# Performance work log

Measured on AMD Instinct MI355X. Metric: run time of the kernel, lower is better.

## Reference

```python
import jax, jax.numpy as jnp
import numpy as np
import math

STEP_SIZE = 1.0


def setup_inputs() -> dict:
    key = jax.random.key(0)
    ks = jax.random.split(key, 6)
    B, L, C, H, O = 4096, 256, 8, 128, 1
    n_int = L - 1
    coeffs = jax.random.normal(ks[0], (B, n_int, 4 * C), dtype=jnp.float32) * 0.1

    def lin(k, i, o):
        kw, kb = jax.random.split(k)
        s = 1.0 / math.sqrt(i)
        W = jax.random.uniform(kw, (i, o), minval=-s, maxval=s, dtype=jnp.float32)
        b = jax.random.uniform(kb, (o,), minval=-s, maxval=s, dtype=jnp.float32)
        return W, b

    W_init, b_init = lin(ks[1], C, H)
    W1, b1 = lin(ks[2], H, H)
    W2, b2 = lin(ks[3], H, H)
    W3, b3 = lin(ks[4], H, H * C)
    W_out, b_out = lin(ks[5], H, O)
    return dict(coeffs=coeffs, W_init=W_init, b_init=b_init, W1=W1, b1=b1,
                W2=W2, b2=b2, W3=W3, b3=b3, W_out=W_out, b_out=b_out)


def reference(coeffs, W_init, b_init, W1, b1, W2, b2, W3, b3, W_out, b_out):
    B, n_int, four_c = coeffs.shape
    C = four_c // 4
    H = W1.shape[0]
    # torchcde CubicSpline coefficient layout: a, b, two_c, three_d
    a, bcoef, two_c, three_d = jnp.split(coeffs, 4, axis=-1)  # each (B, n_int, C)
    knots = jnp.arange(n_int + 1, dtype=coeffs.dtype)  # t = linspace(0, n_int, n_int+1)
    T = float(n_int)

    def X_deriv(t):
        # torchcde _interpret_t: bucketize(t, knots)-1 clamped; here knots uniform
        idx = jnp.clip(jnp.searchsorted(knots, t, side='left') - 1, 0, n_int - 1)
        frac = t - knots[idx]
        return bcoef[:, idx] + (two_c[:, idx] + three_d[:, idx] * frac) * frac  # (B, C)

    def ode_f(t, z):
        # CDEFunc: Linear->Softplus x2, Linear->Tanh, reshape to (B, H, C)
        h = jax.nn.softplus(z @ W1 + b1)
        h = jax.nn.softplus(h @ W2 + b2)
        f = jnp.tanh(h @ W3 + b3).reshape(B, H, C)
        return jnp.einsum('bhc,bc->bh', f, X_deriv(t))  # f(z) @ dX/dt

    # torchdiffeq fixed-grid rk4 with step_size (3/8 rule: rk4_alt_step_func)
    n_steps = int(math.ceil(T / STEP_SIZE))
    ts = jnp.minimum(jnp.arange(n_steps + 1, dtype=coeffs.dtype) * STEP_SIZE, T)
    t0s, dts = ts[:-1], ts[1:] - ts[:-1]

    z0 = a[:, 0] @ W_init + b_init  # X.evaluate(interval[0]) == a at first knot

    def step(z, td):
        t0, dt = td
        k1 = ode_f(t0, z)
        k2 = ode_f(t0 + dt / 3, z + dt * k1 / 3)
        k3 = ode_f(t0 + dt * 2 / 3, z + dt * (k2 - k1 / 3))
        k4 = ode_f(t0 + dt, z + dt * (k1 - k2 + k3))
        return z + dt * (k1 + 3.0 * (k2 + k3) + k4) / 8.0, None

    zT, _ = jax.lax.scan(step, z0, (t0s, dts))
    return zT @ W_out + b_out
```

## Files before the change

### kernel.cpp

```cpp
#include <hip/hip_runtime.h>

#define NINT  255
#define BM    16
#define PITCH 136

typedef __bf16 bf16x8 __attribute__((ext_vector_type(8)));
typedef float  f32x4  __attribute__((ext_vector_type(4)));

#define MFMA(a, b, c) __builtin_amdgcn_mfma_f32_16x16x32_bf16((a), (b), (c), 0, 0, 0)

__device__ __forceinline__ unsigned short f2b(float f) {
    __bf16 b = (__bf16)f;
    return __builtin_bit_cast(unsigned short, b);
}

__device__ __forceinline__ float sp_f(float x) {
    float e = __builtin_amdgcn_exp2f(x * 1.4426950408889634f);
    float y = __builtin_amdgcn_logf(1.0f + e) * 0.6931471805599453f;
    return (x > 80.0f) ? x : y;
}

__device__ __forceinline__ float tanh_f(float x) {
    float e = __builtin_amdgcn_exp2f(x * 2.8853900817779268f);
    float r = __builtin_amdgcn_rcpf(e + 1.0f);
    return fmaf(-2.0f, r, 1.0f);
}

__global__ void prep_frags(const float* __restrict__ W1, const float* __restrict__ W2,
                           const float* __restrict__ W3,
                           unsigned short* __restrict__ W1f, unsigned short* __restrict__ W2f,
                           unsigned short* __restrict__ W3f) {
    const int e = blockIdx.x * 256 + threadIdx.x;
    const int i = e & 7;
    const int l = (e >> 3) & 63;
    const int t = (e >> 9) & 3;
    const int n = e >> 11;
    const int k = 32 * t + ((l >> 4) & 3) * 8 + i;
    const int c = l & 15;
    if (e < 16384) {
        W1f[e] = f2b(W1[k * 128 + 16 * n + c]);
        W2f[e] = f2b(W2[k * 128 + 16 * n + c]);
    }
    W3f[e] = f2b(W3[k * 1024 + 16 * n + c]);
}

#define RK_UPDATE(ST, JL)                                                        \
{                                                                                \
    float znew;                                                                  \
    if (ST == 0)      { k1r[JL] = p; znew = zb[JL] + p * (1.0f/3.0f); }          \
    else if (ST == 1) { k2r[JL] = p; znew = zb[JL] + p - k1r[JL] * (1.0f/3.0f); }\
    else if (ST == 2) { k3r[JL] = p; znew = zb[JL] + k1r[JL] - k2r[JL] + p; }    \
    else { zb[JL] = fmaf(k1r[JL] + 3.0f*(k2r[JL] + k3r[JL]) + p, 0.125f, zb[JL]); znew = zb[JL]; } \
    if ((g & 1) == 0)                                                            \
        Zs[l15 * PITCH + 32 * JL + h2wb] = f2b(znew);                            \
}

#define STAGE_BODY(ST)                                                           \
{                                                                                \
    if (w < 8) {                                                                 \
        bf16x8 a0[4];                                                            \
        _Pragma("unroll") for (int t = 0; t < 4; ++t)                            \
            a0[t] = *(const bf16x8*)(Zs + l15 * PITCH + t * 32 + koff);          \
        f32x4 h1 = {b1r, b1r, b1r, b1r};                                         \
        _Pragma("unroll") for (int t = 0; t < 4; ++t)                            \
            h1 = MFMA(a0[t], w12r[t], h1);                                       \
        _Pragma("unroll") for (int t = 0; t < 4; ++t)                            \
            w12r[t] = w2v[(w * 4 + t) * 64 + l];               \
        _Pragma("unroll") for (int i = 0; i < 4; ++i)                            \
            H1s[(g * 4 + i) * PITCH + 16 * w + l15] = f2b(sp_f(h1[i]));          \
    }                                                                            \
    __syncthreads();                                                             \
    if (w < 8) {                                                                 \
        bf16x8 a1[4];                                                            \
        _Pragma("unroll") for (int t = 0; t < 4; ++t)                            \
            a1[t] = *(const bf16x8*)(H1s + l15 * PITCH + t * 32 + koff);         \
        f32x4 h2 = {b2r, b2r, b2r, b2r};                                         \
        _Pragma("unroll") for (int t = 0; t < 4; ++t)                            \
            h2 = MFMA(a1[t], w12r[t], h2);                                       \
        _Pragma("unroll") for (int t = 0; t < 4; ++t)                            \
            w12r[t] = w1v[(w * 4 + t) * 64 + l];            \
        _Pragma("unroll") for (int i = 0; i < 4; ++i)                            \
            H2s[(g * 4 + i) * PITCH + 16 * w + l15] = f2b(sp_f(h2[i]));          \
    }                                                                            \
    __syncthreads();                                                             \
    {                                                                            \
        bf16x8 bfr[4];                                                           \
        _Pragma("unroll") for (int t = 0; t < 4; ++t)                            \
            bfr[t] = *(const bf16x8*)(H2s + l15 * PITCH + t * 32 + koff);        \
        const f32x4 xdv = *(const f32x4*)&Xds[par][ST][l15][chB];                \
                                           \
        {                                                                        \
            f32x4 acc0 = *(const f32x4*)&b3s[16 * w + 4 * g];                    \
            f32x4 acc1 = *(const f32x4*)&b3s[16 * (16 + w) + 4 * g];             \
            _Pragma("unroll") for (int t = 0; t < 4; ++t) {                      \
                acc0 = MFMA(w3g[0][t], bfr[t], acc0);                            \
                acc1 = MFMA(w3g[1][t], bfr[t], acc1);                            \
            }                                                                    \
            float p;                                                             \
            p = 0.0f;                                                            \
            _Pragma("unroll") for (int i = 0; i < 4; ++i)                        \
                p = fmaf(tanh_f(acc0[i]), xdv[i], p);                            \
            p += __shfl_xor(p, 16, 64);                                          \
            RK_UPDATE(ST, 0)                                                     \
            p = 0.0f;                                                            \
            _Pragma("unroll") for (int i = 0; i < 4; ++i)                        \
                p = fmaf(tanh_f(acc1[i]), xdv[i], p);                            \
            p += __shfl_xor(p, 16, 64);                                          \
            RK_UPDATE(ST, 1)                                                     \
        }                                                                        \
                     \
        {                                                                        \
            f32x4 acc0 = *(const f32x4*)&b3s[16 * (32 + w) + 4 * g];             \
            f32x4 acc1 = *(const f32x4*)&b3s[16 * (48 + w) + 4 * g];             \
            _Pragma("unroll") for (int t = 0; t < 4; ++t) {                      \
                acc0 = MFMA(w3lv[(w * 4 + t) * 64 + l], bfr[t], acc0);           \
                acc1 = MFMA(w3lv[((16 + w) * 4 + t) * 64 + l], bfr[t], acc1);    \
            }                                                                    \
            float p;                                                             \
            p = 0.0f;                                                            \
            _Pragma("unroll") for (int i = 0; i < 4; ++i)                        \
                p = fmaf(tanh_f(acc0[i]), xdv[i], p);                            \
            p += __shfl_xor(p, 16, 64);                                          \
            RK_UPDATE(ST, 2)                                                     \
            p = 0.0f;                                                            \
            _Pragma("unroll") for (int i = 0; i < 4; ++i)                        \
                p = fmaf(tanh_f(acc1[i]), xdv[i], p);                            \
            p += __shfl_xor(p, 16, 64);                                          \
            RK_UPDATE(ST, 3)                                                     \
        }                                                                        \
    }                                                                            \
    __syncthreads();                                                             \
}

__global__ __launch_bounds__(1024, 4)
void cde_mfma(const float* __restrict__ coeffs,
              const float* __restrict__ W_init, const float* __restrict__ b_init,
              const float* __restrict__ b1, const float* __restrict__ b2,
              const float* __restrict__ b3,
              const float* __restrict__ W_out, const float* __restrict__ b_out,
              const unsigned short* __restrict__ w1f, const unsigned short* __restrict__ w2f,
              const unsigned short* __restrict__ w3f,
              float* __restrict__ out)
{
    __shared__ __align__(16) unsigned short W3l_lds[65536];
    __shared__ __align__(16) unsigned short Zs [BM * PITCH];
    __shared__ __align__(16) unsigned short H1s[BM * PITCH];
    __shared__ __align__(16) unsigned short H2s[BM * PITCH];
    __shared__ __align__(16) float b3s[1024];
    __shared__ __align__(16) float Xds[2][4][16][8];
    __shared__ __align__(16) float Outp[32][16];

    const int tid     = threadIdx.x;
    const int rowbase = blockIdx.x * BM;
    const int l       = tid & 63;
    const int w       = tid >> 6;
    const int l15     = l & 15;
    const int g       = (l >> 4) & 3;
    const int hb      = g >> 1;
    const int koff    = g * 8;
    const int chB     = 4 * (g & 1);
    const int h2wb    = 2 * w + hb;

    for (int k4 = tid; k4 < 8192; k4 += 1024)
        ((uint4*)W3l_lds)[k4] = ((const uint4*)(w3f + 32 * 2048))[k4];
    b3s[tid] = b3[tid];

    const bf16x8* w1v = (const bf16x8*)w1f;
    const bf16x8* w2v = (const bf16x8*)w2f;
    const bf16x8* w3v = (const bf16x8*)w3f;
    bf16x8 w3g[2][4];
    #pragma unroll
    for (int jl = 0; jl < 2; ++jl)
        #pragma unroll
        for (int t = 0; t < 4; ++t)
            w3g[jl][t] = w3v[((16 * jl + w) * 4 + t) * 64 + l];

    bf16x8 w12r[4];
    float b1r = 0.0f, b2r = 0.0f;
    if (w < 8) {
        #pragma unroll
        for (int t = 0; t < 4; ++t)
            w12r[t] = w1v[(w * 4 + t) * 64 + l];
        b1r = b1[16 * w + l15];
        b2r = b2[16 * w + l15];
    }

    float zb[4], k1r[4], k2r[4], k3r[4];
    {
        const float* ap = coeffs + (size_t)(rowbase + l15) * (NINT * 32);
        float av[8];
        #pragma unroll
        for (int c = 0; c < 8; ++c) av[c] = ap[c];
        #pragma unroll
        for (int jl = 0; jl < 4; ++jl) {
            const int h = 32 * jl + h2wb;
            float z = b_init[h];
            #pragma unroll
            for (int c = 0; c < 8; ++c) z = fmaf(av[c], W_init[c * 128 + h], z);
            zb[jl] = z;
            if ((g & 1) == 0) Zs[l15 * PITCH + h] = f2b(z);
        }
    }

    const bf16x8* w3lv = (const bf16x8*)W3l_lds;
    __syncthreads();

    #pragma unroll 1
    for (int step = 0; step < NINT; ++step) {
        const int par = step & 1;
        if (tid < 128) {
            const int m = tid >> 3, c = tid & 7;
            const float* cp = coeffs + (size_t)(rowbase + m) * (NINT * 32);
            float s1;
            if (step == 0) s1 = cp[8 + c];
            else {
                const int i0 = (step - 1) * 32;
                s1 = cp[i0 + 8 + c] + cp[i0 + 16 + c] + cp[i0 + 24 + c];
            }
            const int ik = step * 32;
            const float bB = cp[ik + 8 + c];
            const float tc = cp[ik + 16 + c];
            const float td = cp[ik + 24 + c];
            Xds[par][0][m][c] = s1;
            Xds[par][1][m][c] = bB + (tc + td * (1.0f/3.0f)) * (1.0f/3.0f);
            Xds[par][2][m][c] = bB + (tc + td * (2.0f/3.0f)) * (2.0f/3.0f);
            Xds[par][3][m][c] = bB + tc + td;
        }

        STAGE_BODY(0)
        STAGE_BODY(1)
        STAGE_BODY(2)
        STAGE_BODY(3)
    }

    if ((g & 1) == 0) {
        float prt = 0.0f;
        #pragma unroll
        for (int jl = 0; jl < 4; ++jl)
            prt = fmaf(zb[jl], W_out[32 * jl + h2wb], prt);
        Outp[h2wb][l15] = prt;
    }
    __syncthreads();
    if (tid < 16) {
        float s = b_out[0];
        #pragma unroll
        for (int p = 0; p < 32; ++p) s += Outp[p][tid];
        out[rowbase + tid] = s;
    }
}

extern "C" void kernel_launch(void* const* d_in, const int* in_sizes, int n_in,
                              void* d_out, int out_size, void* d_ws, size_t ws_size,
                              hipStream_t stream) {
    const float* coeffs = (const float*)d_in[0];
    const float* W_init = (const float*)d_in[1];
    const float* b_init = (const float*)d_in[2];
    const float* W1     = (const float*)d_in[3];
    const float* b1     = (const float*)d_in[4];
    const float* W2     = (const float*)d_in[5];
    const float* b2     = (const float*)d_in[6];
    const float* W3     = (const float*)d_in[7];
    const float* b3     = (const float*)d_in[8];
    const float* W_out  = (const float*)d_in[9];
    const float* b_out  = (const float*)d_in[10];
    float* outp = (float*)d_out;

    unsigned short* w1f = (unsigned short*)d_ws;
    unsigned short* w2f = w1f + 16384;
    unsigned short* w3f = w2f + 16384;

    hipLaunchKernelGGL(prep_frags, dim3(512), dim3(256), 0, stream, W1, W2, W3, w1f, w2f, w3f);
    hipLaunchKernelGGL(cde_mfma, dim3(4096 / BM), dim3(1024), 0, stream,
                       coeffs, W_init, b_init, b1, b2, b3, W_out, b_out,
                       w1f, w2f, w3f, outp);
}
```

Baseline: 3.069 ms.

## Shrink block to 12 waves and redistribute W3 tiles unevenly across waves

The block drops from 16 to 12 wavefronts (768 threads). The 64 W3 output tiles are now spread across the waves, with waves 0-3 handling 6 tiles and the rest 5. Each wave holds 3 register-resident W3 fragment groups instead of 2; tiles 32 and up still read from LDS. This is meant to cut per-block scheduling and barrier overhead and raise per-wave work, at the cost of load imbalance, more registers per wave, and fewer waves to hide latency.

Measured after the change: 2.907 ms. 5.3% less time.

```diff
diff --git a/kernel.cpp b/kernel.cpp
--- a/kernel.cpp
+++ b/kernel.cpp
@@ -44,15 +44,15 @@
     W3f[e] = f2b(W3[k * 1024 + 16 * n + c]);
 }
 
-#define RK_UPDATE(ST, JL)                                                        \
+#define RK_UPDATE(ST, T, TILE)                                                   \
 {                                                                                \
     float znew;                                                                  \
-    if (ST == 0)      { k1r[JL] = p; znew = zb[JL] + p * (1.0f/3.0f); }          \
-    else if (ST == 1) { k2r[JL] = p; znew = zb[JL] + p - k1r[JL] * (1.0f/3.0f); }\
-    else if (ST == 2) { k3r[JL] = p; znew = zb[JL] + k1r[JL] - k2r[JL] + p; }    \
-    else { zb[JL] = fmaf(k1r[JL] + 3.0f*(k2r[JL] + k3r[JL]) + p, 0.125f, zb[JL]); znew = zb[JL]; } \
+    if (ST == 0)      { k1r[T] = p; znew = zb[T] + p * (1.0f/3.0f); }            \
+    else if (ST == 1) { k2r[T] = p; znew = zb[T] + p - k1r[T] * (1.0f/3.0f); }   \
+    else if (ST == 2) { k3r[T] = p; znew = zb[T] + k1r[T] - k2r[T] + p; }        \
+    else { zb[T] = fmaf(k1r[T] + 3.0f*(k2r[T] + k3r[T]) + p, 0.125f, zb[T]); znew = zb[T]; } \
     if ((g & 1) == 0)                                                            \
-        Zs[l15 * PITCH + 32 * JL + h2wb] = f2b(znew);                            \
+        Zs[l15 * PITCH + 2 * (TILE) + hb] = f2b(znew);                           \
 }
 
 #define STAGE_BODY(ST)                                                           \
@@ -88,51 +88,30 @@
         _Pragma("unroll") for (int t = 0; t < 4; ++t)                            \
             bfr[t] = *(const bf16x8*)(H2s + l15 * PITCH + t * 32 + koff);        \
         const f32x4 xdv = *(const f32x4*)&Xds[par][ST][l15][chB];                \
-                                           \
-        {                                                                        \
-            f32x4 acc0 = *(const f32x4*)&b3s[16 * w + 4 * g];                    \
-            f32x4 acc1 = *(const f32x4*)&b3s[16 * (16 + w) + 4 * g];             \
-            _Pragma("unroll") for (int t = 0; t < 4; ++t) {                      \
-                acc0 = MFMA(w3g[0][t], bfr[t], acc0);                            \
-                acc1 = MFMA(w3g[1][t], bfr[t], acc1);                            \
+        _Pragma("unroll")                                                        \
+        for (int t = 0; t < 6; ++t) {                                            \
+            if (t < ntl) {                                                       \
+                const int tile = 12 * t + w;                                     \
+                f32x4 acc = *(const f32x4*)&b3s[16 * tile + 4 * g];              \
+                if (tile < 32) {                                                 \
+                    _Pragma("unroll") for (int tt = 0; tt < 4; ++tt)             \
+                        acc = MFMA(w3g[t][tt], bfr[tt], acc);                    \
+                } else {                                                         \
+                    _Pragma("unroll") for (int tt = 0; tt < 4; ++tt)             \
+                        acc = MFMA(w3lv[((tile - 32) * 4 + tt) * 64 + l], bfr[tt], acc); \
+                }                                                                \
+                float p = 0.0f;                                                  \
+                _Pragma("unroll") for (int i = 0; i < 4; ++i)                    \
+                    p = fmaf(tanh_f(acc[i]), xdv[i], p);                         \
+                p += __shfl_xor(p, 16, 64);                                      \
+                RK_UPDATE(ST, t, tile)                                           \
             }                                                                    \
-            float p;                                                             \
-            p = 0.0f;                                                            \
-            _Pragma("unroll") for (int i = 0; i < 4; ++i)                        \
-                p = fmaf(tanh_f(acc0[i]), xdv[i], p);                            \
-            p += __shfl_xor(p, 16, 64);                                          \
-            RK_UPDATE(ST, 0)                                                     \
-            p = 0.0f;                                                            \
-            _Pragma("unroll") for (int i = 0; i < 4; ++i)                        \
-                p = fmaf(tanh_f(acc1[i]), xdv[i], p);                            \
-            p += __shfl_xor(p, 16, 64);                                          \
-            RK_UPDATE(ST, 1)                                                     \
-        }                                                                        \
-                     \
-        {                                                                        \
-            f32x4 acc0 = *(const f32x4*)&b3s[16 * (32 + w) + 4 * g];             \
-            f32x4 acc1 = *(const f32x4*)&b3s[16 * (48 + w) + 4 * g];             \
-            _Pragma("unroll") for (int t = 0; t < 4; ++t) {                      \
-                acc0 = MFMA(w3lv[(w * 4 + t) * 64 + l], bfr[t], acc0);           \
-                acc1 = MFMA(w3lv[((16 + w) * 4 + t) * 64 + l], bfr[t], acc1);    \
-            }                                                                    \
-            float p;                                                             \
-            p = 0.0f;                                                            \
-            _Pragma("unroll") for (int i = 0; i < 4; ++i)                        \
-                p = fmaf(tanh_f(acc0[i]), xdv[i], p);                            \
-            p += __shfl_xor(p, 16, 64);                                          \
-            RK_UPDATE(ST, 2)                                                     \
-            p = 0.0f;                                                            \
-            _Pragma("unroll") for (int i = 0; i < 4; ++i)                        \
-                p = fmaf(tanh_f(acc1[i]), xdv[i], p);                            \
-            p += __shfl_xor(p, 16, 64);                                          \
-            RK_UPDATE(ST, 3)                                                     \
         }                                                                        \
     }                                                                            \
     __syncthreads();                                                             \
 }
 
-__global__ __launch_bounds__(1024, 4)
+__global__ __launch_bounds__(768, 3)
 void cde_mfma(const float* __restrict__ coeffs,
               const float* __restrict__ W_init, const float* __restrict__ b_init,
               const float* __restrict__ b1, const float* __restrict__ b2,
@@ -148,7 +127,7 @@
     __shared__ __align__(16) unsigned short H2s[BM * PITCH];
     __shared__ __align__(16) float b3s[1024];
     __shared__ __align__(16) float Xds[2][4][16][8];
-    __shared__ __align__(16) float Outp[32][16];
+    __shared__ __align__(16) float Outp[24][16];
 
     const int tid     = threadIdx.x;
     const int rowbase = blockIdx.x * BM;
@@ -159,21 +138,21 @@
     const int hb      = g >> 1;
     const int koff    = g * 8;
     const int chB     = 4 * (g & 1);
-    const int h2wb    = 2 * w + hb;
-
-    for (int k4 = tid; k4 < 8192; k4 += 1024)
+    const int ntl     = (w < 4) ? 6 : 5;
+
+    for (int k4 = tid; k4 < 8192; k4 += 768)
         ((uint4*)W3l_lds)[k4] = ((const uint4*)(w3f + 32 * 2048))[k4];
-    b3s[tid] = b3[tid];
+    for (int k = tid; k < 1024; k += 768) b3s[k] = b3[k];
 
     const bf16x8* w1v = (const bf16x8*)w1f;
     const bf16x8* w2v = (const bf16x8*)w2f;
     const bf16x8* w3v = (const bf16x8*)w3f;
-    bf16x8 w3g[2][4];
+    bf16x8 w3g[3][4];
     #pragma unroll
-    for (int jl = 0; jl < 2; ++jl)
-        #pragma unroll
-        for (int t = 0; t < 4; ++t)
-            w3g[jl][t] = w3v[((16 * jl + w) * 4 + t) * 64 + l];
+    for (int t = 0; t < 3; ++t)
+        #pragma unroll
+        for (int tt = 0; tt < 4; ++tt)
+            w3g[t][tt] = w3v[((12 * t + w) * 4 + tt) * 64 + l];
 
     bf16x8 w12r[4];
     float b1r = 0.0f, b2r = 0.0f;
@@ -185,20 +164,22 @@
         b2r = b2[16 * w + l15];
     }
 
-    float zb[4], k1r[4], k2r[4], k3r[4];
+    float zb[6], k1r[6], k2r[6], k3r[6];
     {
         const float* ap = coeffs + (size_t)(rowbase + l15) * (NINT * 32);
         float av[8];
         #pragma unroll
         for (int c = 0; c < 8; ++c) av[c] = ap[c];
         #pragma unroll
-        for (int jl = 0; jl < 4; ++jl) {
-            const int h = 32 * jl + h2wb;
-            float z = b_init[h];
-            #pragma unroll
-            for (int c = 0; c < 8; ++c) z = fmaf(av[c], W_init[c * 128 + h], z);
-            zb[jl] = z;
-            if ((g & 1) == 0) Zs[l15 * PITCH + h] = f2b(z);
+        for (int t = 0; t < 6; ++t) {
+            if (t < ntl) {
+                const int h = 2 * (12 * t + w) + hb;
+                float z = b_init[h];
+                #pragma unroll
+                for (int c = 0; c < 8; ++c) z = fmaf(av[c], W_init[c * 128 + h], z);
+                zb[t] = z;
+                if ((g & 1) == 0) Zs[l15 * PITCH + h] = f2b(z);
+            }
         }
     }
 
@@ -236,15 +217,16 @@
     if ((g & 1) == 0) {
         float prt = 0.0f;
         #pragma unroll
-        for (int jl = 0; jl < 4; ++jl)
-            prt = fmaf(zb[jl], W_out[32 * jl + h2wb], prt);
-        Outp[h2wb][l15] = prt;
+        for (int t = 0; t < 6; ++t)
+            if (t < ntl)
+                prt = fmaf(zb[t], W_out[2 * (12 * t + w) + hb], prt);
+        Outp[2 * w + hb][l15] = prt;
     }
     __syncthreads();
     if (tid < 16) {
         float s = b_out[0];
         #pragma unroll
-        for (int p = 0; p < 32; ++p) s += Outp[p][tid];
+        for (int p = 0; p < 24; ++p) s += Outp[p][tid];
         out[rowbase + tid] = s;
     }
 }
@@ -270,7 +252,7 @@
     unsigned short* w3f = w2f + 16384;
 
     hipLaunchKernelGGL(prep_frags, dim3(512), dim3(256), 0, stream, W1, W2, W3, w1f, w2f, w3f);
-    hipLaunchKernelGGL(cde_mfma, dim3(4096 / BM), dim3(1024), 0, stream,
+    hipLaunchKernelGGL(cde_mfma, dim3(4096 / BM), dim3(768), 0, stream,
                        coeffs, W_init, b_init, b1, b2, b3, W_out, b_out,
                        w1f, w2f, w3f, outp);
 }
```
